# Kernel tuning notes

Hardware: AMD Instinct MI355X
Metric: run time of the kernel (lower is better)

The kernel has to match this reference:

```python
import jax, jax.numpy as jnp
import numpy as np

# --- static config (matches init_kwargs) ---
C = 384        # channels
H = 8          # num_heads
HD = C // H    # head_dim = 48
K = 1024       # patch_size (window)
BASE = 100.0   # rope_freq
MAX_POS = 4096
GRID_SIZE = 0.02
LN_EPS = 1e-5


def _interleave8(x, y, z):
    """Morton-interleave the low 8 bits of x,y,z -> 24-bit code (int32)."""
    key = jnp.zeros_like(x)
    for i in range(8):
        m = 1 << i
        key = key | ((x & m) << (2 * i + 2)) | ((y & m) << (2 * i + 1)) | ((z & m) << (2 * i))
    return key


def _serialize_points(xyz):
    """xyz: (B,3,N) -> (order (B,N) int32, grid (B,N,3) int32). Z-order sort."""
    pts = jnp.transpose(xyz, (0, 2, 1))                       # (B,N,3)
    grid = ((pts - pts.min(axis=1, keepdims=True)) / GRID_SIZE).astype(jnp.int32)
    grid = jnp.clip(grid, 0, 65535)
    gx, gy, gz = grid[..., 0], grid[..., 1], grid[..., 2]
    lo = _interleave8(gx & 255, gy & 255, gz & 255)           # low 24 bits of Morton code
    hi = _interleave8((gx >> 8) & 255, (gy >> 8) & 255, (gz >> 8) & 255)  # high word
    # 48-bit Morton order == lexsort with hi as primary key, lo secondary
    order = jax.vmap(lambda l, h: jnp.lexsort((l, h)))(lo, hi)
    return order.astype(jnp.int32), grid


def _rope_tables(d):
    inv_freq = 1.0 / (BASE ** (jnp.arange(0, d, 2, dtype=jnp.float32) / d))
    t = jnp.arange(MAX_POS, dtype=jnp.float32)
    freqs = t[:, None] * inv_freq[None, :]                    # (MAX_POS, d/2)
    freqs = jnp.concatenate([freqs, freqs], axis=-1)          # (MAX_POS, d)
    return jnp.cos(freqs), jnp.sin(freqs)


def _rotate_half(x):
    h = x.shape[-1] // 2
    return jnp.concatenate([-x[..., h:], x[..., :h]], axis=-1)


def _point_rope(tok, pos):
    """tok: (B,H,N,D) with D%3==0; pos: (B,N,3) int grid coords."""
    D = tok.shape[-1]
    d = D // 3
    pos = jnp.clip(pos, 0, MAX_POS - 1)
    cos, sin = _rope_tables(d)
    outs = []
    for axis, ch in enumerate(jnp.split(tok, 3, axis=-1)):
        p = pos[:, :, axis]                                   # (B,N)
        c = cos[p][:, None]                                   # (B,1,N,d)
        s = sin[p][:, None]
        outs.append(ch * c + _rotate_half(ch) * s)
    return jnp.concatenate(outs, axis=-1)


def _layernorm(x, g, b):
    mu = x.mean(axis=-1, keepdims=True)
    var = ((x - mu) ** 2).mean(axis=-1, keepdims=True)
    return (x - mu) * jax.lax.rsqrt(var + LN_EPS) * g + b


def _forward(x, xyz, ln1_g, ln1_b, qkv_w, qkv_b, proj_w, proj_b,
             ln2_g, ln2_b, ffn_w1, ffn_b1, ffn_w2, ffn_b2):
    B, C_, N = x.shape
    order, grid = _serialize_points(xyz)
    x_sorted = jnp.take_along_axis(x, order[:, None, :], axis=2)          # (B,C,N)
    grid_sorted = jnp.take_along_axis(grid, order[:, :, None], axis=1)    # (B,N,3)
    x_t = jnp.transpose(x_sorted, (0, 2, 1))                              # (B,N,C)
    shortcut = x_t
    xn = _layernorm(x_t, ln1_g, ln1_b)
    pad = (K - N % K) % K
    if pad > 0:
        xn = jnp.pad(xn, ((0, 0), (0, pad), (0, 0)))
        grid_sorted = jnp.pad(grid_sorted, ((0, 0), (0, pad), (0, 0)))
    Np = xn.shape[1]
    nw = Np // K
    qkv = (xn @ qkv_w + qkv_b).reshape(B, Np, 3, H, HD)
    q = jnp.transpose(qkv[:, :, 0], (0, 2, 1, 3))                         # (B,H,Np,HD)
    k = jnp.transpose(qkv[:, :, 1], (0, 2, 1, 3))
    v = jnp.transpose(qkv[:, :, 2], (0, 2, 1, 3))
    q = _point_rope(q, grid_sorted)
    k = _point_rope(k, grid_sorted)
    qw = q.reshape(B, H, nw, K, HD)
    kw = k.reshape(B, H, nw, K, HD)
    vw = v.reshape(B, H, nw, K, HD)
    scale = 1.0 / np.sqrt(HD).astype(np.float32)
    scores = jnp.einsum('bhwqd,bhwkd->bhwqk', qw, kw) * scale             # (B,H,nw,K,K)
    attn = jax.nn.softmax(scores, axis=-1)
    out = jnp.einsum('bhwqk,bhwkd->bhwqd', attn, vw)                      # (B,H,nw,K,HD)
    out = jnp.transpose(out, (0, 2, 3, 1, 4)).reshape(B, Np, C)
    out = out[:, :N]
    out = out @ proj_w + proj_b
    x_t = shortcut + out
    x_t = x_t + (jax.nn.gelu(_layernorm(x_t, ln2_g, ln2_b) @ ffn_w1 + ffn_b1,
                             approximate=False) @ ffn_w2 + ffn_b2)
    x_out = jnp.transpose(x_t, (0, 2, 1))                                 # (B,C,N)
    inv_order = jnp.argsort(order, axis=1)
    x_out = jnp.take_along_axis(x_out, inv_order[:, None, :], axis=2)
    return x_out


def setup_inputs() -> dict:
    key = jax.random.key(0)
    ks = jax.random.split(key, 12)
    B, N = 1, 16384
    s = 0.02
    return {
        'x': jax.random.normal(ks[0], (B, C, N), dtype=jnp.float32),
        'xyz': jax.random.uniform(ks[1], (B, 3, N), dtype=jnp.float32),
        'ln1_g': jnp.ones((C,), jnp.float32),
        'ln1_b': jnp.zeros((C,), jnp.float32),
        'qkv_w': jax.random.normal(ks[2], (C, 3 * C), jnp.float32) * s,
        'qkv_b': jnp.zeros((3 * C,), jnp.float32),
        'proj_w': jax.random.normal(ks[3], (C, C), jnp.float32) * s,
        'proj_b': jnp.zeros((C,), jnp.float32),
        'ln2_g': jnp.ones((C,), jnp.float32),
        'ln2_b': jnp.zeros((C,), jnp.float32),
        'ffn_w1': jax.random.normal(ks[4], (C, 4 * C), jnp.float32) * s,
        'ffn_b1': jnp.zeros((4 * C,), jnp.float32),
        'ffn_w2': jax.random.normal(ks[5], (4 * C, C), jnp.float32) * s,
        'ffn_b2': jnp.zeros((C,), jnp.float32),
    }


def reference(x, xyz, ln1_g, ln1_b, qkv_w, qkv_b, proj_w, proj_b,
              ln2_g, ln2_b, ffn_w1, ffn_b1, ffn_w2, ffn_b2):
    return _forward(x, xyz, ln1_g, ln1_b, qkv_w, qkv_b, proj_w, proj_b,
                    ln2_g, ln2_b, ffn_w1, ffn_b1, ffn_w2, ffn_b2)
```

## Files before the change

### kernel.cpp

```cpp
#include <hip/hip_runtime.h>
#include <hip/hip_bf16.h>

typedef unsigned short u16;
typedef unsigned int u32;
typedef unsigned long long u64;
typedef __attribute__((ext_vector_type(8))) short s16x8;
typedef __attribute__((ext_vector_type(4))) short s16x4;
typedef __attribute__((ext_vector_type(8))) unsigned short u16x8;
typedef __attribute__((ext_vector_type(4))) unsigned short u16x4;
typedef __attribute__((ext_vector_type(4))) float fx4;
typedef __attribute__((ext_vector_type(4))) unsigned int ux4;
typedef __attribute__((ext_vector_type(2))) unsigned int ux2;

__device__ __forceinline__ float bf2f(u16 u){ u32 x=((u32)u)<<16; return __builtin_bit_cast(float,x); }
__device__ __forceinline__ u16 f2bf(float f){ u32 x=__builtin_bit_cast(u32,f); return (u16)((x + 0x7FFFu + ((x>>16)&1u))>>16); }
__device__ __forceinline__ u32 cvtpk(float lo, float hi){
  u32 r; asm("v_cvt_pk_bf16_f32 %0, %1, %2" : "=v"(r) : "v"(lo), "v"(hi)); return r;
}

__device__ __forceinline__ s16x8 ld_bf8(const u16* p){
  s16x4 lo = *(const s16x4*)p;
  s16x4 hi = *(const s16x4*)(p+4);
  s16x8 r;
  r[0]=lo[0]; r[1]=lo[1]; r[2]=lo[2]; r[3]=lo[3];
  r[4]=hi[0]; r[5]=hi[1]; r[6]=hi[2]; r[7]=hi[3];
  return r;
}

__device__ __forceinline__ void gload16(const void* g, void* l){
  __builtin_amdgcn_global_load_lds((__attribute__((address_space(1))) void*)g,
                                   (__attribute__((address_space(3))) void*)l, 16, 0, 0);
}

__device__ __forceinline__ u64 spread3(u32 v){
  u64 x = v & 0xFFFFull;
  x = (x | (x<<32)) & 0x001f00000000ffffull;
  x = (x | (x<<16)) & 0x001f0000ff0000ffull;
  x = (x | (x<<8))  & 0x100f00f00f00f00full;
  x = (x | (x<<4))  & 0x10c30c30c30c30c3ull;
  x = (x | (x<<2))  & 0x1249249249249249ull;
  return x;
}

__global__ __launch_bounds__(256) void min3_kernel(const float* __restrict__ xyz, u32* __restrict__ mins, int N)
{
  int i = blockIdx.x*256 + threadIdx.x;
  float v0 = xyz[i], v1 = xyz[N+i], v2 = xyz[2*N+i];
  #pragma unroll
  for (int s=1;s<64;s<<=1){
    v0 = fminf(v0, __shfl_xor(v0,s));
    v1 = fminf(v1, __shfl_xor(v1,s));
    v2 = fminf(v2, __shfl_xor(v2,s));
  }
  if ((threadIdx.x & 63) == 0){
    atomicMin(mins+0, __builtin_bit_cast(u32, v0));
    atomicMin(mins+1, __builtin_bit_cast(u32, v1));
    atomicMin(mins+2, __builtin_bit_cast(u32, v2));
  }
}

__global__ __launch_bounds__(256) void keys_grid_kernel(const float* __restrict__ xyz, const u32* __restrict__ mins,
        u64* __restrict__ keys, int* __restrict__ gridO, int N)
{
  int i = blockIdx.x*256 + threadIdx.x;
  float mx0 = __builtin_bit_cast(float, mins[0]);
  float mx1 = __builtin_bit_cast(float, mins[1]);
  float mx2 = __builtin_bit_cast(float, mins[2]);
  int gx=(int)((xyz[i]-mx0)/0.02f);     gx = gx<0?0:(gx>65535?65535:gx);
  int gy=(int)((xyz[N+i]-mx1)/0.02f);   gy = gy<0?0:(gy>65535?65535:gy);
  int gz=(int)((xyz[2*N+i]-mx2)/0.02f); gz = gz<0?0:(gz>65535?65535:gz);
  gridO[i*3+0]=gx; gridO[i*3+1]=gy; gridO[i*3+2]=gz;
  u64 mort = (spread3((u32)gx)<<2)|(spread3((u32)gy)<<1)|spread3((u32)gz);
  keys[i] = (mort<<14) | (u64)i;
}

__global__ __launch_bounds__(1024) void bsort_kernel(u64* __restrict__ keys)
{
  __shared__ u64 sk[2048];
  int t = threadIdx.x;
  u64* base = keys + (size_t)blockIdx.x*2048;
  sk[t] = base[t]; sk[t+1024] = base[t+1024];
  for (int size=2; size<=2048; size<<=1){
    for (int stride=size>>1; stride>0; stride>>=1){
      __syncthreads();
      int i = 2*t - (t & (stride-1));
      int j = i + stride;
      u64 a = sk[i], b = sk[j];
      bool up = ((i & size) == 0);
      if ((a > b) == up){ sk[i]=b; sk[j]=a; }
    }
  }
  __syncthreads();
  base[t] = sk[t]; base[t+1024] = sk[t+1024];
}

template<bool FINAL>
__global__ __launch_bounds__(256) void merge_kernel(const u64* __restrict__ src, u64* __restrict__ dst,
        int* __restrict__ order, int L, int N)
{
  int gt = blockIdx.x*256 + threadIdx.x;
  int d0 = gt*8;
  if (d0 >= N) return;
  int pair = d0 / (2*L);
  int base = pair*2*L;
  int ld = d0 - base;
  const u64* A = src + base;
  const u64* B = A + L;
  int lo = ld > L ? ld - L : 0;
  int hi = ld < L ? ld : L;
  while (lo < hi){
    int mid = (lo+hi)>>1;
    if (A[mid] <= B[ld-1-mid]) lo = mid+1; else hi = mid;
  }
  int i = lo, j = ld - lo;
  u64* out = dst + base + ld;
  int* oout = order + base + ld;
  u64 a = (i < L) ? A[i] : ~0ull;
  u64 b = (j < L) ? B[j] : ~0ull;
  #pragma unroll
  for (int e=0;e<8;e++){
    u64 v;
    if (a <= b){ v = a; i++; a = (i<L)?A[i]:~0ull; }
    else       { v = b; j++; b = (j<L)?B[j]:~0ull; }
    out[e] = v;
    if (FINAL) oout[e] = (int)(v & 16383ull);
  }
}

__global__ __launch_bounds__(256) void wtrans4_kernel(const float* __restrict__ qkv_w, const float* __restrict__ proj_w,
    const float* __restrict__ w1, const float* __restrict__ w2,
    u16* __restrict__ qkv_wT, u16* __restrict__ proj_wT, u16* __restrict__ w1T, u16* __restrict__ w2T)
{
  __shared__ float tl[32][33];
  int bid = blockIdx.x;
  const float* W; u16* Wt; int K, Nc, lb;
  if (bid < 432)      { W=qkv_w;  Wt=qkv_wT;  K=384;  Nc=1152; lb=bid; }
  else if (bid < 576) { W=proj_w; Wt=proj_wT; K=384;  Nc=384;  lb=bid-432; }
  else if (bid < 1152){ W=w1;     Wt=w1T;     K=384;  Nc=1536; lb=bid-576; }
  else                { W=w2;     Wt=w2T;     K=1536; Nc=384;  lb=bid-1152; }
  int nb = Nc/32;
  int n0 = (lb % nb)*32;
  int k0 = (lb / nb)*32;
  int t=threadIdx.x; int r=t>>5, c=t&31;
  #pragma unroll
  for (int p=0;p<4;p++) tl[p*8+r][c] = W[(size_t)(k0+p*8+r)*Nc + n0+c];
  __syncthreads();
  #pragma unroll
  for (int p=0;p<4;p++) Wt[(size_t)(n0+p*8+r)*K + k0+c] = f2bf(tl[c][p*8+r]);
}

__global__ __launch_bounds__(256) void ln32_kernel(const float* __restrict__ x, const float* __restrict__ g,
     const float* __restrict__ b, u16* __restrict__ xn, int N)
{
  extern __shared__ char dsm[];
  float* tile = (float*)dsm;
  int n0 = blockIdx.x*32;
  int t = threadIdx.x;
  int tok32 = t&31, cg = t>>5;
  #pragma unroll 8
  for (int p=0;p<48;p++){
    int cc = p*8 + cg;
    tile[tok32*388 + cc] = x[(size_t)cc*N + n0 + tok32];
  }
  __syncthreads();
  int tok = t>>3, part = t&7;
  const float* row = tile + tok*388 + part*48;
  float s=0.f;
  #pragma unroll
  for (int j=0;j<48;j++) s += row[j];
  s += __shfl_xor(s,1); s += __shfl_xor(s,2); s += __shfl_xor(s,4);
  float mu = s*(1.0f/384.0f);
  float vr=0.f;
  #pragma unroll
  for (int j=0;j<48;j++){ float d=row[j]-mu; vr += d*d; }
  vr += __shfl_xor(vr,1); vr += __shfl_xor(vr,2); vr += __shfl_xor(vr,4);
  float rs = rsqrtf(vr*(1.0f/384.0f) + 1e-5f);
  u16* dst = xn + (size_t)(n0+tok)*384 + part*48;
  #pragma unroll
  for (int q=0;q<6;q++){
    float v[8];
    #pragma unroll
    for (int j=0;j<8;j++){
      int c = part*48 + q*8 + j;
      v[j] = (row[q*8+j]-mu)*rs*g[c] + b[c];
    }
    ux4 o;
    o[0]=cvtpk(v[0],v[1]); o[1]=cvtpk(v[2],v[3]); o[2]=cvtpk(v[4],v[5]); o[3]=cvtpk(v[6],v[7]);
    *(ux4*)(dst + q*8) = o;
  }
}

__device__ __forceinline__ float gelu_f(float v){
  return 0.5f*v*(1.0f + erff(v*0.7071067811865475f));
}

template<int EPI>
__global__ __launch_bounds__(256) void gemm128_kernel(const u16* __restrict__ A, const u16* __restrict__ Bt,
    const float* __restrict__ bias, u16* __restrict__ outB, float* __restrict__ outF,
    const float* __restrict__ res, int M, int Nout, int K)
{
  __shared__ u16 Al[128*64];
  __shared__ u16 Bl[128*64];
  int nmt = M>>7;
  int m0 = (blockIdx.x % nmt)<<7;
  int n0 = (blockIdx.x / nmt)<<7;
  int t = threadIdx.x, lane=t&63, wv=t>>6, wr=wv>>1, wc=wv&1;
  int fr = lane&15, fg = lane>>4;
  fx4 acc[4][4];
  #pragma unroll
  for (int i=0;i<4;i++)
  #pragma unroll
  for (int j=0;j<4;j++) acc[i][j]=(fx4){0.f,0.f,0.f,0.f};
  int srow = wv*32 + (lane>>3);
  int swz  = ((lane&7) ^ ((lane>>3)&7)) * 8;
  const u16* ApL = A  + (size_t)(m0+srow)*K + swz;
  const u16* BpL = Bt + (size_t)(n0+srow)*K + swz;
  u16* AlW = Al + wv*2048 + lane*8;
  u16* BlW = Bl + wv*2048 + lane*8;
  const u16* a_base = Al + (wr*64+fr)*64;
  const u16* b_base = Bl + (wc*64+fr)*64;
  int swr = fr & 7;
  for (int k0=0;k0<K;k0+=64){
    #pragma unroll
    for (int i=0;i<4;i++){
      gload16(ApL + k0 + (size_t)i*8*K, AlW + i*512);
      gload16(BpL + k0 + (size_t)i*8*K, BlW + i*512);
    }
    __syncthreads();
    #pragma unroll
    for (int ks=0;ks<2;ks++){
      int soff = (((ks*4+fg) ^ swr) << 3);
      s16x8 a[4], b[4];
      #pragma unroll
      for (int mi=0;mi<4;mi++) a[mi] = *(const s16x8*)(a_base + mi*1024 + soff);
      #pragma unroll
      for (int ni=0;ni<4;ni++) b[ni] = *(const s16x8*)(b_base + ni*1024 + soff);
      #pragma unroll
      for (int mi=0;mi<4;mi++)
      #pragma unroll
      for (int ni=0;ni<4;ni++)
        acc[mi][ni] = __builtin_amdgcn_mfma_f32_16x16x32_bf16(a[mi], b[ni], acc[mi][ni], 0,0,0);
    }
    __syncthreads();
  }
  if (EPI==0 || EPI==1){
    #pragma unroll
    for (int mi=0;mi<4;mi++)
    #pragma unroll
    for (int ni=0;ni<4;ni++){
      int c = n0 + wc*64 + ni*16 + fr;
      float bi = bias[c];
      int mb = m0 + wr*64 + mi*16 + fg*4;
      #pragma unroll
      for (int j=0;j<4;j++){
        float vv = acc[mi][ni][j] + bi;
        if (EPI==1) vv = gelu_f(vv);
        outB[(size_t)(mb+j)*Nout + c] = f2bf(vv);
      }
    }
  } else {
    #pragma unroll
    for (int mi=0;mi<4;mi++)
    #pragma unroll
    for (int ni=0;ni<4;ni++){
      int c = n0 + wc*64 + ni*16 + fr;
      float bi = bias[c];
      size_t idx = (size_t)c*M + m0 + wr*64 + mi*16 + fg*4;
      fx4 r4 = *(const fx4*)(res + idx);
      fx4 o;
      #pragma unroll
      for (int j=0;j<4;j++) o[j] = acc[mi][ni][j] + bi + r4[j];
      *(fx4*)(outF + idx) = o;
    }
  }
}

#define LOG2_100_O8 0.8304820237218405f

__global__ __launch_bounds__(256) void rope_kernel(const u16* __restrict__ qkv, const int* __restrict__ order,
    const int* __restrict__ gridO, u16* __restrict__ Qp, u16* __restrict__ Kp, u16* __restrict__ Vp, int N)
{
  __shared__ float csm[64][24][2];
  __shared__ int origs[64];
  int i0 = blockIdx.x<<6;
  int t = threadIdx.x;
  if (t<64) origs[t] = order[i0+t];
  __syncthreads();
  for (int idx=t; idx<64*24; idx+=256){
    int tok = idx/24, slot = idx - tok*24;
    int a = slot>>3, fi = slot&7;
    int pos = gridO[(size_t)origs[tok]*3 + a];
    pos = pos<0?0:(pos>4095?4095:pos);
    float invf = __builtin_amdgcn_exp2f(-(float)fi * LOG2_100_O8);
    float ang = (float)pos * invf;
    csm[tok][slot][0] = __cosf(ang);
    csm[tok][slot][1] = __sinf(ang);
  }
  __syncthreads();
  int tok = t&63;
  int i = i0 + tok;
  const u16* src = qkv + (size_t)origs[tok]*1152;
  for (int h=t>>6; h<8; h+=4){
    size_t dst = ((size_t)h*N + i)*48;
    #pragma unroll
    for (int a=0;a<3;a++){
      u16x8 qa = *(const u16x8*)(src + h*48 + a*16);
      u16x8 qb = *(const u16x8*)(src + h*48 + a*16 + 8);
      u16x8 ka = *(const u16x8*)(src + 384 + h*48 + a*16);
      u16x8 kb = *(const u16x8*)(src + 384 + h*48 + a*16 + 8);
      float oqa[8], oqb[8], oka[8], okb[8];
      #pragma unroll
      for (int j=0;j<8;j++){
        float c0 = csm[tok][a*8+j][0], s0 = csm[tok][a*8+j][1];
        float ql = bf2f(qa[j]), qh = bf2f(qb[j]);
        float kl = bf2f(ka[j]), kh = bf2f(kb[j]);
        oqa[j] = ql*c0 - qh*s0;
        oqb[j] = qh*c0 + ql*s0;
        oka[j] = kl*c0 - kh*s0;
        okb[j] = kh*c0 + kl*s0;
      }
      ux4 OQa, OQb, OKa, OKb;
      #pragma unroll
      for (int p=0;p<4;p++){
        OQa[p]=cvtpk(oqa[2*p],oqa[2*p+1]);
        OQb[p]=cvtpk(oqb[2*p],oqb[2*p+1]);
        OKa[p]=cvtpk(oka[2*p],oka[2*p+1]);
        OKb[p]=cvtpk(okb[2*p],okb[2*p+1]);
      }
      *(ux4*)(Qp + dst + a*16) = OQa;
      *(ux4*)(Qp + dst + a*16 + 8) = OQb;
      *(ux4*)(Kp + dst + a*16) = OKa;
      *(ux4*)(Kp + dst + a*16 + 8) = OKb;
      u16x8 va = *(const u16x8*)(src + 768 + h*48 + a*16);
      u16x8 vb = *(const u16x8*)(src + 768 + h*48 + a*16 + 8);
      *(u16x8*)(Vp + dst + a*16) = va;
      *(u16x8*)(Vp + dst + a*16 + 8) = vb;
    }
  }
}

#define ATTN_SCALE 0.14433756729740643f
#define E2SCALE 0.2082354550504211f
#define DEFER_RAW 55.0f
#define KSTRIDE 68

__global__ __launch_bounds__(512) void attn5_kernel(const u16* __restrict__ Qp, const u16* __restrict__ Kp,
    const u16* __restrict__ Vp, const int* __restrict__ order, u16* __restrict__ attn, int N, int nw)
{
  __shared__ u16 Kl[64*KSTRIDE];
  __shared__ u16 Vl[48*KSTRIDE];
  __shared__ u16 Pl[8][32*KSTRIDE];
  int b = blockIdx.x;
  int hw = b & 127;
  int qc = b >> 7;
  int w = hw % nw, h = hw / nw;
  int t = threadIdx.x, lane = t&63, wv = t>>6;
  int fr = lane & 15, fg = lane >> 4;
  size_t base = ((size_t)h*N + (size_t)w*1024);
  int q0 = qc*256 + wv*32;
  bool kact = t < 384;
  int krow = t/6, kc = t - krow*6;
  const u16* ksrc = Kp + (base + krow)*48 + kc*8;
  u16* kdst = Kl + krow*KSTRIDE + kc*8;
  int s2 = t - 128;
  bool vact = t >= 128;
  int vrow = s2/6, vc = s2 - vrow*6;
  const u16* vsrc = Vp + (base + vrow)*48 + vc*8;
  int vkey = vrow ^ (vc<<3);
  if (t < 256){ ux2 z = {0,0}; *(ux2*)&Kl[(t>>2)*KSTRIDE + 48 + (t&3)*4] = z; }
  s16x8 qf[2][2];
  s16x8 zf = {0,0,0,0,0,0,0,0};
  #pragma unroll
  for (int n=0;n<2;n++){
    const u16* qrow = Qp + (base + q0 + n*16 + fr)*48;
    qf[n][0] = ld_bf8(qrow + fg*8);
    qf[n][1] = (fg < 2) ? ld_bf8(qrow + 32 + fg*8) : zf;
  }

  float m0r = -3.4e38f, m1r = -3.4e38f;
  float ls0 = 0.f, ls1 = 0.f;
  fx4 o00=(fx4){0.f,0.f,0.f,0.f}, o01=o00, o02=o00, o10=o00, o11=o00, o12=o00;
  u16* pl = Pl[wv];
  ux4 kreg = {0,0,0,0}, vreg = {0,0,0,0};
  if (kact) kreg = *(const ux4*)ksrc;
  if (vact) vreg = *(const ux4*)vsrc;

  for (int c=0;c<16;c++){
    __syncthreads();
    if (kact){
      ux2 lo; lo[0]=kreg[0]; lo[1]=kreg[1];
      ux2 hi; hi[0]=kreg[2]; hi[1]=kreg[3];
      *(ux2*)kdst = lo; *(ux2*)(kdst+4) = hi;
    }
    if (vact){
      u16* vcp = Vl + vkey;
      vcp[(vc*8+0)*KSTRIDE] = (u16)vreg[0];
      vcp[(vc*8+1)*KSTRIDE] = (u16)(vreg[0]>>16);
      vcp[(vc*8+2)*KSTRIDE] = (u16)vreg[1];
      vcp[(vc*8+3)*KSTRIDE] = (u16)(vreg[1]>>16);
      vcp[(vc*8+4)*KSTRIDE] = (u16)vreg[2];
      vcp[(vc*8+5)*KSTRIDE] = (u16)(vreg[2]>>16);
      vcp[(vc*8+6)*KSTRIDE] = (u16)vreg[3];
      vcp[(vc*8+7)*KSTRIDE] = (u16)(vreg[3]>>16);
    }
    __syncthreads();
    if (c < 15){
      if (kact) kreg = *(const ux4*)(ksrc + (size_t)(c+1)*3072);
      if (vact) vreg = *(const ux4*)(vsrc + (size_t)(c+1)*3072);
    }
    fx4 s0[4], s1v[4];
    #pragma unroll
    for (int m=0;m<4;m++){
      s0[m]=(fx4){0.f,0.f,0.f,0.f}; s1v[m]=s0[m];
      #pragma unroll
      for (int s=0;s<2;s++){
        s16x8 af = ld_bf8(Kl + (m*16+fr)*KSTRIDE + s*32 + fg*8);
        s0[m]  = __builtin_amdgcn_mfma_f32_16x16x32_bf16(af, qf[0][s], s0[m],  0,0,0);
        s1v[m] = __builtin_amdgcn_mfma_f32_16x16x32_bf16(af, qf[1][s], s1v[m], 0,0,0);
      }
    }
    float pm0 = -3.4e38f, pm1 = -3.4e38f;
    #pragma unroll
    for (int m=0;m<4;m++)
    #pragma unroll
    for (int j=0;j<4;j++){ pm0 = fmaxf(pm0, s0[m][j]); pm1 = fmaxf(pm1, s1v[m][j]); }
    pm0 = fmaxf(pm0, __shfl_xor(pm0,16)); pm0 = fmaxf(pm0, __shfl_xor(pm0,32));
    pm1 = fmaxf(pm1, __shfl_xor(pm1,16)); pm1 = fmaxf(pm1, __shfl_xor(pm1,32));
    if (!__all((pm0 <= m0r + DEFER_RAW) & (pm1 <= m1r + DEFER_RAW))){
      float nm0 = fmaxf(m0r, pm0), nm1 = fmaxf(m1r, pm1);
      float f0 = __builtin_amdgcn_exp2f((m0r - nm0)*E2SCALE);
      float f1 = __builtin_amdgcn_exp2f((m1r - nm1)*E2SCALE);
      ls0 *= f0; ls1 *= f1;
      m0r = nm0; m1r = nm1;
      #pragma unroll
      for (int j=0;j<4;j++){
        float g0 = __shfl(f0, fg*4+j);
        float g1 = __shfl(f1, fg*4+j);
        o00[j]*=g0; o01[j]*=g0; o02[j]*=g0;
        o10[j]*=g1; o11[j]*=g1; o12[j]*=g1;
      }
    }
    #pragma unroll
    for (int m=0;m<4;m++){
      float e0[4], e1[4];
      #pragma unroll
      for (int j=0;j<4;j++){
        e0[j] = __builtin_amdgcn_exp2f((s0[m][j]-m0r)*E2SCALE);
        e1[j] = __builtin_amdgcn_exp2f((s1v[m][j]-m1r)*E2SCALE);
        ls0 += e0[j]; ls1 += e1[j];
      }
      ux2 P0, P1;
      P0[0]=cvtpk(e0[0],e0[1]); P0[1]=cvtpk(e0[2],e0[3]);
      P1[0]=cvtpk(e1[0],e1[1]); P1[1]=cvtpk(e1[2],e1[3]);
      *(ux2*)&pl[(fr)*KSTRIDE + m*16 + fg*4]      = P0;
      *(ux2*)&pl[(16+fr)*KSTRIDE + m*16 + fg*4]   = P1;
    }
    #pragma unroll
    for (int s=0;s<2;s++){
      s16x8 pa0 = ld_bf8(pl + fr*KSTRIDE + s*32 + fg*8);
      s16x8 pa1 = ld_bf8(pl + (16+fr)*KSTRIDE + s*32 + fg*8);
      int kb = s*32 + fg*8;
      s16x8 vb0 = ld_bf8(Vl + (fr)*KSTRIDE    + (kb ^ ((fr)&56)));
      s16x8 vb1 = ld_bf8(Vl + (16+fr)*KSTRIDE + (kb ^ ((16+fr)&56)));
      s16x8 vb2 = ld_bf8(Vl + (32+fr)*KSTRIDE + (kb ^ ((32+fr)&56)));
      o00 = __builtin_amdgcn_mfma_f32_16x16x32_bf16(pa0, vb0, o00, 0,0,0);
      o01 = __builtin_amdgcn_mfma_f32_16x16x32_bf16(pa0, vb1, o01, 0,0,0);
      o02 = __builtin_amdgcn_mfma_f32_16x16x32_bf16(pa0, vb2, o02, 0,0,0);
      o10 = __builtin_amdgcn_mfma_f32_16x16x32_bf16(pa1, vb0, o10, 0,0,0);
      o11 = __builtin_amdgcn_mfma_f32_16x16x32_bf16(pa1, vb1, o11, 0,0,0);
      o12 = __builtin_amdgcn_mfma_f32_16x16x32_bf16(pa1, vb2, o12, 0,0,0);
    }
  }
  ls0 += __shfl_xor(ls0,16); ls0 += __shfl_xor(ls0,32);
  ls1 += __shfl_xor(ls1,16); ls1 += __shfl_xor(ls1,32);
  float r0 = 1.0f/ls0, r1 = 1.0f/ls1;
  const int* ord = order + w*1024 + q0;
  #pragma unroll
  for (int j=0;j<4;j++){
    float inv0 = __shfl(r0, fg*4+j);
    float inv1 = __shfl(r1, fg*4+j);
    int orig0 = ord[fg*4+j];
    u16* dst0 = attn + (size_t)orig0*384 + h*48;
    dst0[fr]      = f2bf(o00[j]*inv0);
    dst0[16+fr]   = f2bf(o01[j]*inv0);
    dst0[32+fr]   = f2bf(o02[j]*inv0);
    int orig1 = ord[16 + fg*4+j];
    u16* dst1 = attn + (size_t)orig1*384 + h*48;
    dst1[fr]      = f2bf(o10[j]*inv1);
    dst1[16+fr]   = f2bf(o11[j]*inv1);
    dst1[32+fr]   = f2bf(o12[j]*inv1);
  }
}

extern "C" void kernel_launch(void* const* d_in, const int* in_sizes, int n_in,
                              void* d_out, int out_size, void* d_ws, size_t ws_size,
                              hipStream_t stream)
{
  (void)n_in; (void)out_size; (void)ws_size;
  const float* x     = (const float*)d_in[0];
  const float* xyz   = (const float*)d_in[1];
  const float* ln1_g = (const float*)d_in[2];
  const float* ln1_b = (const float*)d_in[3];
  const float* qkv_w = (const float*)d_in[4];
  const float* qkv_b = (const float*)d_in[5];
  const float* proj_w= (const float*)d_in[6];
  const float* proj_b= (const float*)d_in[7];
  const float* ln2_g = (const float*)d_in[8];
  const float* ln2_b = (const float*)d_in[9];
  const float* ffn_w1= (const float*)d_in[10];
  const float* ffn_b1= (const float*)d_in[11];
  const float* ffn_w2= (const float*)d_in[12];
  const float* ffn_b2= (const float*)d_in[13];
  int N = in_sizes[0]/384;
  int nw = N/1024;
  char* wsp = (char*)d_ws;
  size_t off = 0;
  auto alloc = [&](size_t bytes)->char*{ char* p = wsp + off; off = (off + bytes + 255) & ~(size_t)255; return p; };
  int*  order   = (int*)alloc((size_t)N*4);
  int*  gridO   = (int*)alloc((size_t)N*12);
  u32*  mins    = (u32*)alloc(256);
  u64*  keysA   = (u64*)alloc((size_t)N*8);
  u64*  keysB   = (u64*)alloc((size_t)N*8);
  u16*  qkv_wT  = (u16*)alloc((size_t)1152*384*2);
  u16*  proj_wT = (u16*)alloc((size_t)384*384*2);
  u16*  w1T     = (u16*)alloc((size_t)1536*384*2);
  u16*  w2T     = (u16*)alloc((size_t)384*1536*2);
  u16*  xn      = (u16*)alloc((size_t)N*384*2);
  u16*  Qp      = (u16*)alloc((size_t)N*48*8*2);
  u16*  Kp      = (u16*)alloc((size_t)N*48*8*2);
  u16*  Vp      = (u16*)alloc((size_t)N*48*8*2);
  u16*  qkvb    = (u16*)alloc((size_t)N*1152*2);
  float* y1     = (float*)alloc((size_t)N*384*4);
  u16*  attn    = xn;
  u16*  xn2     = qkvb;
  u16*  mid     = xn;
  float* outF = (float*)d_out;

  hipMemsetAsync(mins, 0xFF, 12, stream);
  min3_kernel<<<N/256, 256, 0, stream>>>(xyz, mins, N);
  keys_grid_kernel<<<N/256, 256, 0, stream>>>(xyz, mins, keysA, gridO, N);
  bsort_kernel<<<N/2048, 1024, 0, stream>>>(keysA);
  merge_kernel<false><<<N/2048, 256, 0, stream>>>(keysA, keysB, order, 2048, N);
  merge_kernel<false><<<N/2048, 256, 0, stream>>>(keysB, keysA, order, 4096, N);
  merge_kernel<true><<<N/2048, 256, 0, stream>>>(keysA, keysB, order, 8192, N);

  wtrans4_kernel<<<1728, 256, 0, stream>>>(qkv_w, proj_w, ffn_w1, ffn_w2, qkv_wT, proj_wT, w1T, w2T);
  ln32_kernel<<<N/32, 256, 32*388*4, stream>>>(x, ln1_g, ln1_b, xn, N);
  gemm128_kernel<0><<<(N/128)*(1152/128), 256, 0, stream>>>(xn, qkv_wT, qkv_b, qkvb, nullptr, nullptr, N, 1152, 384);
  rope_kernel<<<N/64, 256, 0, stream>>>(qkvb, order, gridO, Qp, Kp, Vp, N);
  attn5_kernel<<<8*nw*4, 512, 0, stream>>>(Qp, Kp, Vp, order, attn, N, nw);
  gemm128_kernel<2><<<(N/128)*(384/128), 256, 0, stream>>>(attn, proj_wT, proj_b, nullptr, y1, x, N, 384, 384);
  ln32_kernel<<<N/32, 256, 32*388*4, stream>>>(y1, ln2_g, ln2_b, xn2, N);
  gemm128_kernel<1><<<(N/128)*(1536/128), 256, 0, stream>>>(xn2, w1T, ffn_b1, mid, nullptr, nullptr, N, 1536, 384);
  gemm128_kernel<2><<<(N/128)*(384/128), 256, 0, stream>>>(mid, w2T, ffn_b2, nullptr, outF, y1, N, 384, 1536);
}
```

Baseline: 291.9 us.

## Fuse sort into cooperative kernel, pre-transpose V, store residual in bf16

Replaces the six sort-stage launches (memset, min, keys, bitonic, three merges) with one 8-block cooperative kernel that uses grid syncs. The rope kernel now writes V transposed per window, so attention loads V tiles with vector stores instead of scattered transposing LDS writes. The intermediate residual y1 is stored as bf16 rather than fp32, which halves its traffic but loses precision. s_setprio hints are added around the MFMA blocks. The merge stages now run on only 8 workgroups, which limits parallelism, and the strided transposed V writes in rope may be costly.

```diff
diff --git a/kernel.cpp b/kernel.cpp
--- a/kernel.cpp
+++ b/kernel.cpp
@@ -1,5 +1,8 @@
 #include <hip/hip_runtime.h>
 #include <hip/hip_bf16.h>
+#include <hip/hip_cooperative_groups.h>
+
+namespace cg = cooperative_groups;
 
 typedef unsigned short u16;
 typedef unsigned int u32;
@@ -42,65 +45,10 @@
   return x;
 }
 
-__global__ __launch_bounds__(256) void min3_kernel(const float* __restrict__ xyz, u32* __restrict__ mins, int N)
-{
-  int i = blockIdx.x*256 + threadIdx.x;
-  float v0 = xyz[i], v1 = xyz[N+i], v2 = xyz[2*N+i];
-  #pragma unroll
-  for (int s=1;s<64;s<<=1){
-    v0 = fminf(v0, __shfl_xor(v0,s));
-    v1 = fminf(v1, __shfl_xor(v1,s));
-    v2 = fminf(v2, __shfl_xor(v2,s));
-  }
-  if ((threadIdx.x & 63) == 0){
-    atomicMin(mins+0, __builtin_bit_cast(u32, v0));
-    atomicMin(mins+1, __builtin_bit_cast(u32, v1));
-    atomicMin(mins+2, __builtin_bit_cast(u32, v2));
-  }
-}
-
-__global__ __launch_bounds__(256) void keys_grid_kernel(const float* __restrict__ xyz, const u32* __restrict__ mins,
-        u64* __restrict__ keys, int* __restrict__ gridO, int N)
-{
-  int i = blockIdx.x*256 + threadIdx.x;
-  float mx0 = __builtin_bit_cast(float, mins[0]);
-  float mx1 = __builtin_bit_cast(float, mins[1]);
-  float mx2 = __builtin_bit_cast(float, mins[2]);
-  int gx=(int)((xyz[i]-mx0)/0.02f);     gx = gx<0?0:(gx>65535?65535:gx);
-  int gy=(int)((xyz[N+i]-mx1)/0.02f);   gy = gy<0?0:(gy>65535?65535:gy);
-  int gz=(int)((xyz[2*N+i]-mx2)/0.02f); gz = gz<0?0:(gz>65535?65535:gz);
-  gridO[i*3+0]=gx; gridO[i*3+1]=gy; gridO[i*3+2]=gz;
-  u64 mort = (spread3((u32)gx)<<2)|(spread3((u32)gy)<<1)|spread3((u32)gz);
-  keys[i] = (mort<<14) | (u64)i;
-}
-
-__global__ __launch_bounds__(1024) void bsort_kernel(u64* __restrict__ keys)
-{
-  __shared__ u64 sk[2048];
-  int t = threadIdx.x;
-  u64* base = keys + (size_t)blockIdx.x*2048;
-  sk[t] = base[t]; sk[t+1024] = base[t+1024];
-  for (int size=2; size<=2048; size<<=1){
-    for (int stride=size>>1; stride>0; stride>>=1){
-      __syncthreads();
-      int i = 2*t - (t & (stride-1));
-      int j = i + stride;
-      u64 a = sk[i], b = sk[j];
-      bool up = ((i & size) == 0);
-      if ((a > b) == up){ sk[i]=b; sk[j]=a; }
-    }
-  }
-  __syncthreads();
-  base[t] = sk[t]; base[t+1024] = sk[t+1024];
-}
-
-template<bool FINAL>
-__global__ __launch_bounds__(256) void merge_kernel(const u64* __restrict__ src, u64* __restrict__ dst,
-        int* __restrict__ order, int L, int N)
-{
-  int gt = blockIdx.x*256 + threadIdx.x;
-  int d0 = gt*8;
-  if (d0 >= N) return;
+__device__ __forceinline__ void merge2(const u64* __restrict__ src, u64* __restrict__ dst,
+        int* __restrict__ order, int L, int gt)
+{
+  int d0 = gt*2;
   int pair = d0 / (2*L);
   int base = pair*2*L;
   int ld = d0 - base;
@@ -113,18 +61,72 @@
     if (A[mid] <= B[ld-1-mid]) lo = mid+1; else hi = mid;
   }
   int i = lo, j = ld - lo;
-  u64* out = dst + base + ld;
-  int* oout = order + base + ld;
-  u64 a = (i < L) ? A[i] : ~0ull;
-  u64 b = (j < L) ? B[j] : ~0ull;
-  #pragma unroll
-  for (int e=0;e<8;e++){
+  #pragma unroll
+  for (int e=0;e<2;e++){
+    u64 a = (i < L) ? A[i] : ~0ull;
+    u64 b = (j < L) ? B[j] : ~0ull;
     u64 v;
-    if (a <= b){ v = a; i++; a = (i<L)?A[i]:~0ull; }
-    else       { v = b; j++; b = (j<L)?B[j]:~0ull; }
-    out[e] = v;
-    if (FINAL) oout[e] = (int)(v & 16383ull);
-  }
+    if (a <= b){ v = a; i++; } else { v = b; j++; }
+    dst[base+ld+e] = v;
+    if (order) order[base+ld+e] = (int)(v & 16383ull);
+  }
+}
+
+__global__ __launch_bounds__(1024) void sortc_kernel(const float* __restrict__ xyz,
+    float* __restrict__ minsW, u64* __restrict__ keysA, u64* __restrict__ keysB,
+    int* __restrict__ order, int* __restrict__ gridO, int N)
+{
+  cg::grid_group gg = cg::this_grid();
+  __shared__ u64 sk[2048];
+  __shared__ float red[3][16];
+  int t = threadIdx.x, bid = blockIdx.x;
+  int lane = t&63, wv = t>>6;
+  float m0=3.4e38f,m1=3.4e38f,m2=3.4e38f;
+  for (int i = bid*1024 + t; i < N; i += 8192){
+    m0=fminf(m0,xyz[i]); m1=fminf(m1,xyz[N+i]); m2=fminf(m2,xyz[2*N+i]);
+  }
+  #pragma unroll
+  for (int s=1;s<64;s<<=1){
+    m0=fminf(m0,__shfl_xor(m0,s));
+    m1=fminf(m1,__shfl_xor(m1,s));
+    m2=fminf(m2,__shfl_xor(m2,s));
+  }
+  if (lane==0){ red[0][wv]=m0; red[1][wv]=m1; red[2][wv]=m2; }
+  __syncthreads();
+  if (t<3){ float m=red[t][0]; for(int i=1;i<16;i++) m=fminf(m,red[t][i]); minsW[bid*3+t]=m; }
+  gg.sync();
+  float mn0=minsW[0], mn1=minsW[1], mn2=minsW[2];
+  for (int bb=1;bb<8;bb++){
+    mn0=fminf(mn0,minsW[bb*3+0]); mn1=fminf(mn1,minsW[bb*3+1]); mn2=fminf(mn2,minsW[bb*3+2]);
+  }
+  for (int i = bid*2048 + t; i < bid*2048 + 2048; i += 1024){
+    int gx=(int)((xyz[i]-mn0)/0.02f);     gx = gx<0?0:(gx>65535?65535:gx);
+    int gy=(int)((xyz[N+i]-mn1)/0.02f);   gy = gy<0?0:(gy>65535?65535:gy);
+    int gz=(int)((xyz[2*N+i]-mn2)/0.02f); gz = gz<0?0:(gz>65535?65535:gz);
+    gridO[i*3+0]=gx; gridO[i*3+1]=gy; gridO[i*3+2]=gz;
+    u64 mort = (spread3((u32)gx)<<2)|(spread3((u32)gy)<<1)|spread3((u32)gz);
+    sk[i - bid*2048] = (mort<<14) | (u64)i;
+  }
+  for (int size=2; size<=2048; size<<=1){
+    for (int stride=size>>1; stride>0; stride>>=1){
+      __syncthreads();
+      int i = 2*t - (t & (stride-1));
+      int j = i + stride;
+      u64 a = sk[i], b = sk[j];
+      bool up = ((i & size) == 0);
+      if ((a > b) == up){ sk[i]=b; sk[j]=a; }
+    }
+  }
+  __syncthreads();
+  keysA[bid*2048 + t] = sk[t];
+  keysA[bid*2048 + 1024 + t] = sk[t+1024];
+  gg.sync();
+  int gt = bid*1024 + t;
+  merge2(keysA, keysB, nullptr, 2048, gt);
+  gg.sync();
+  merge2(keysB, keysA, nullptr, 4096, gt);
+  gg.sync();
+  merge2(keysA, keysB, order, 8192, gt);
 }
 
 __global__ __launch_bounds__(256) void wtrans4_kernel(const float* __restrict__ qkv_w, const float* __restrict__ proj_w,
@@ -149,18 +151,22 @@
   for (int p=0;p<4;p++) Wt[(size_t)(n0+p*8+r)*K + k0+c] = f2bf(tl[c][p*8+r]);
 }
 
-__global__ __launch_bounds__(256) void ln32_kernel(const float* __restrict__ x, const float* __restrict__ g,
+template<bool BF16IN>
+__global__ __launch_bounds__(256) void ln32_kernel(const void* __restrict__ xin, const float* __restrict__ g,
      const float* __restrict__ b, u16* __restrict__ xn, int N)
 {
   extern __shared__ char dsm[];
   float* tile = (float*)dsm;
   int n0 = blockIdx.x*32;
   int t = threadIdx.x;
-  int tok32 = t&31, cg = t>>5;
+  int tok32 = t&31, cg2 = t>>5;
   #pragma unroll 8
   for (int p=0;p<48;p++){
-    int cc = p*8 + cg;
-    tile[tok32*388 + cc] = x[(size_t)cc*N + n0 + tok32];
+    int cc = p*8 + cg2;
+    float v;
+    if (BF16IN) v = bf2f(((const u16*)xin)[(size_t)cc*N + n0 + tok32]);
+    else        v = ((const float*)xin)[(size_t)cc*N + n0 + tok32];
+    tile[tok32*388 + cc] = v;
   }
   __syncthreads();
   int tok = t>>3, part = t&7;
@@ -197,7 +203,7 @@
 template<int EPI>
 __global__ __launch_bounds__(256) void gemm128_kernel(const u16* __restrict__ A, const u16* __restrict__ Bt,
     const float* __restrict__ bias, u16* __restrict__ outB, float* __restrict__ outF,
-    const float* __restrict__ res, int M, int Nout, int K)
+    const float* __restrict__ resF, const u16* __restrict__ resB, int M, int Nout, int K)
 {
   __shared__ u16 Al[128*64];
   __shared__ u16 Bl[128*64];
@@ -258,7 +264,7 @@
         outB[(size_t)(mb+j)*Nout + c] = f2bf(vv);
       }
     }
-  } else {
+  } else if (EPI==2){
     #pragma unroll
     for (int mi=0;mi<4;mi++)
     #pragma unroll
@@ -266,10 +272,26 @@
       int c = n0 + wc*64 + ni*16 + fr;
       float bi = bias[c];
       size_t idx = (size_t)c*M + m0 + wr*64 + mi*16 + fg*4;
-      fx4 r4 = *(const fx4*)(res + idx);
+      fx4 r4 = *(const fx4*)(resF + idx);
+      ux2 p;
+      p[0] = cvtpk(acc[mi][ni][0]+bi+r4[0], acc[mi][ni][1]+bi+r4[1]);
+      p[1] = cvtpk(acc[mi][ni][2]+bi+r4[2], acc[mi][ni][3]+bi+r4[3]);
+      *(ux2*)(outB + idx) = p;
+    }
+  } else {
+    #pragma unroll
+    for (int mi=0;mi<4;mi++)
+    #pragma unroll
+    for (int ni=0;ni<4;ni++){
+      int c = n0 + wc*64 + ni*16 + fr;
+      float bi = bias[c];
+      size_t idx = (size_t)c*M + m0 + wr*64 + mi*16 + fg*4;
+      ux2 rb = *(const ux2*)(resB + idx);
       fx4 o;
-      #pragma unroll
-      for (int j=0;j<4;j++) o[j] = acc[mi][ni][j] + bi + r4[j];
+      o[0] = acc[mi][ni][0] + bi + bf2f((u16)rb[0]);
+      o[1] = acc[mi][ni][1] + bi + bf2f((u16)(rb[0]>>16));
+      o[2] = acc[mi][ni][2] + bi + bf2f((u16)rb[1]);
+      o[3] = acc[mi][ni][3] + bi + bf2f((u16)(rb[1]>>16));
       *(fx4*)(outF + idx) = o;
     }
   }
@@ -278,11 +300,12 @@
 #define LOG2_100_O8 0.8304820237218405f
 
 __global__ __launch_bounds__(256) void rope_kernel(const u16* __restrict__ qkv, const int* __restrict__ order,
-    const int* __restrict__ gridO, u16* __restrict__ Qp, u16* __restrict__ Kp, u16* __restrict__ Vp, int N)
+    const int* __restrict__ gridO, u16* __restrict__ Qp, u16* __restrict__ Kp, u16* __restrict__ Vt, int N)
 {
   __shared__ float csm[64][24][2];
   __shared__ int origs[64];
   int i0 = blockIdx.x<<6;
+  int nw = N>>10;
   int t = threadIdx.x;
   if (t<64) origs[t] = order[i0+t];
   __syncthreads();
@@ -299,9 +322,12 @@
   __syncthreads();
   int tok = t&63;
   int i = i0 + tok;
+  int wdx = i >> 10;
+  int kw = i & 1023;
   const u16* src = qkv + (size_t)origs[tok]*1152;
   for (int h=t>>6; h<8; h+=4){
     size_t dst = ((size_t)h*N + i)*48;
+    u16* vt = Vt + (((size_t)h*nw + wdx)*48)*1024 + kw;
     #pragma unroll
     for (int a=0;a<3;a++){
       u16x8 qa = *(const u16x8*)(src + h*48 + a*16);
@@ -333,8 +359,11 @@
       *(ux4*)(Kp + dst + a*16 + 8) = OKb;
       u16x8 va = *(const u16x8*)(src + 768 + h*48 + a*16);
       u16x8 vb = *(const u16x8*)(src + 768 + h*48 + a*16 + 8);
-      *(u16x8*)(Vp + dst + a*16) = va;
-      *(u16x8*)(Vp + dst + a*16 + 8) = vb;
+      #pragma unroll
+      for (int j=0;j<8;j++){
+        vt[(size_t)(a*16+j)*1024]   = va[j];
+        vt[(size_t)(a*16+8+j)*1024] = vb[j];
+      }
     }
   }
 }
@@ -344,8 +373,8 @@
 #define DEFER_RAW 55.0f
 #define KSTRIDE 68
 
-__global__ __launch_bounds__(512) void attn5_kernel(const u16* __restrict__ Qp, const u16* __restrict__ Kp,
-    const u16* __restrict__ Vp, const int* __restrict__ order, u16* __restrict__ attn, int N, int nw)
+__global__ __launch_bounds__(512) void attn6_kernel(const u16* __restrict__ Qp, const u16* __restrict__ Kp,
+    const u16* __restrict__ Vt, const int* __restrict__ order, u16* __restrict__ attn, int N, int nw)
 {
   __shared__ u16 Kl[64*KSTRIDE];
   __shared__ u16 Vl[48*KSTRIDE];
@@ -357,6 +386,7 @@
   int t = threadIdx.x, lane = t&63, wv = t>>6;
   int fr = lane & 15, fg = lane >> 4;
   size_t base = ((size_t)h*N + (size_t)w*1024);
+  size_t vbase = ((size_t)h*nw + w)*48;
   int q0 = qc*256 + wv*32;
   bool kact = t < 384;
   int krow = t/6, kc = t - krow*6;
@@ -364,9 +394,9 @@
   u16* kdst = Kl + krow*KSTRIDE + kc*8;
   int s2 = t - 128;
   bool vact = t >= 128;
-  int vrow = s2/6, vc = s2 - vrow*6;
-  const u16* vsrc = Vp + (base + vrow)*48 + vc*8;
-  int vkey = vrow ^ (vc<<3);
+  int vrow = s2>>3, vcg = (s2&7)*8;
+  const u16* vsrc = Vt + (vbase + vrow)*1024 + vcg;
+  u16* vdst = Vl + vrow*KSTRIDE + vcg;
   if (t < 256){ ux2 z = {0,0}; *(ux2*)&Kl[(t>>2)*KSTRIDE + 48 + (t&3)*4] = z; }
   s16x8 qf[2][2];
   s16x8 zf = {0,0,0,0,0,0,0,0};
@@ -393,22 +423,17 @@
       *(ux2*)kdst = lo; *(ux2*)(kdst+4) = hi;
     }
     if (vact){
-      u16* vcp = Vl + vkey;
-      vcp[(vc*8+0)*KSTRIDE] = (u16)vreg[0];
-      vcp[(vc*8+1)*KSTRIDE] = (u16)(vreg[0]>>16);
-      vcp[(vc*8+2)*KSTRIDE] = (u16)vreg[1];
-      vcp[(vc*8+3)*KSTRIDE] = (u16)(vreg[1]>>16);
-      vcp[(vc*8+4)*KSTRIDE] = (u16)vreg[2];
-      vcp[(vc*8+5)*KSTRIDE] = (u16)(vreg[2]>>16);
-      vcp[(vc*8+6)*KSTRIDE] = (u16)vreg[3];
-      vcp[(vc*8+7)*KSTRIDE] = (u16)(vreg[3]>>16);
+      ux2 lo; lo[0]=vreg[0]; lo[1]=vreg[1];
+      ux2 hi; hi[0]=vreg[2]; hi[1]=vreg[3];
+      *(ux2*)vdst = lo; *(ux2*)(vdst+4) = hi;
     }
     __syncthreads();
     if (c < 15){
       if (kact) kreg = *(const ux4*)(ksrc + (size_t)(c+1)*3072);
-      if (vact) vreg = *(const ux4*)(vsrc + (size_t)(c+1)*3072);
+      if (vact) vreg = *(const ux4*)(vsrc + (size_t)(c+1)*64);
     }
     fx4 s0[4], s1v[4];
+    __builtin_amdgcn_s_setprio(1);
     #pragma unroll
     for (int m=0;m<4;m++){
       s0[m]=(fx4){0.f,0.f,0.f,0.f}; s1v[m]=s0[m];
@@ -419,11 +444,14 @@
         s1v[m] = __builtin_amdgcn_mfma_f32_16x16x32_bf16(af, qf[1][s], s1v[m], 0,0,0);
       }
     }
+    __builtin_amdgcn_s_setprio(0);
     float pm0 = -3.4e38f, pm1 = -3.4e38f;
     #pragma unroll
-    for (int m=0;m<4;m++)
-    #pragma unroll
-    for (int j=0;j<4;j++){ pm0 = fmaxf(pm0, s0[m][j]); pm1 = fmaxf(pm1, s1v[m][j]); }
+    for (int m=0;m<4;m++){
+      float a0 = fmaxf(fmaxf(s0[m][0],s0[m][1]), fmaxf(s0[m][2],s0[m][3]));
+      float a1 = fmaxf(fmaxf(s1v[m][0],s1v[m][1]), fmaxf(s1v[m][2],s1v[m][3]));
+      pm0 = fmaxf(pm0, a0); pm1 = fmaxf(pm1, a1);
+    }
     pm0 = fmaxf(pm0, __shfl_xor(pm0,16)); pm0 = fmaxf(pm0, __shfl_xor(pm0,32));
     pm1 = fmaxf(pm1, __shfl_xor(pm1,16)); pm1 = fmaxf(pm1, __shfl_xor(pm1,32));
     if (!__all((pm0 <= m0r + DEFER_RAW) & (pm1 <= m1r + DEFER_RAW))){
@@ -455,14 +483,15 @@
       *(ux2*)&pl[(fr)*KSTRIDE + m*16 + fg*4]      = P0;
       *(ux2*)&pl[(16+fr)*KSTRIDE + m*16 + fg*4]   = P1;
     }
+    __builtin_amdgcn_s_setprio(1);
     #pragma unroll
     for (int s=0;s<2;s++){
-      s16x8 pa0 = ld_bf8(pl + fr*KSTRIDE + s*32 + fg*8);
-      s16x8 pa1 = ld_bf8(pl + (16+fr)*KSTRIDE + s*32 + fg*8);
       int kb = s*32 + fg*8;
-      s16x8 vb0 = ld_bf8(Vl + (fr)*KSTRIDE    + (kb ^ ((fr)&56)));
-      s16x8 vb1 = ld_bf8(Vl + (16+fr)*KSTRIDE + (kb ^ ((16+fr)&56)));
-      s16x8 vb2 = ld_bf8(Vl + (32+fr)*KSTRIDE + (kb ^ ((32+fr)&56)));
+      s16x8 pa0 = ld_bf8(pl + fr*KSTRIDE + kb);
+      s16x8 pa1 = ld_bf8(pl + (16+fr)*KSTRIDE + kb);
+      s16x8 vb0 = ld_bf8(Vl + (fr)*KSTRIDE    + kb);
+      s16x8 vb1 = ld_bf8(Vl + (16+fr)*KSTRIDE + kb);
+      s16x8 vb2 = ld_bf8(Vl + (32+fr)*KSTRIDE + kb);
       o00 = __builtin_amdgcn_mfma_f32_16x16x32_bf16(pa0, vb0, o00, 0,0,0);
       o01 = __builtin_amdgcn_mfma_f32_16x16x32_bf16(pa0, vb1, o01, 0,0,0);
       o02 = __builtin_amdgcn_mfma_f32_16x16x32_bf16(pa0, vb2, o02, 0,0,0);
@@ -470,6 +499,7 @@
       o11 = __builtin_amdgcn_mfma_f32_16x16x32_bf16(pa1, vb1, o11, 0,0,0);
       o12 = __builtin_amdgcn_mfma_f32_16x16x32_bf16(pa1, vb2, o12, 0,0,0);
     }
+    __builtin_amdgcn_s_setprio(0);
   }
   ls0 += __shfl_xor(ls0,16); ls0 += __shfl_xor(ls0,32);
   ls1 += __shfl_xor(ls1,16); ls1 += __shfl_xor(ls1,32);
@@ -518,7 +548,7 @@
   auto alloc = [&](size_t bytes)->char*{ char* p = wsp + off; off = (off + bytes + 255) & ~(size_t)255; return p; };
   int*  order   = (int*)alloc((size_t)N*4);
   int*  gridO   = (int*)alloc((size_t)N*12);
-  u32*  mins    = (u32*)alloc(256);
+  float* minsW  = (float*)alloc(256);
   u64*  keysA   = (u64*)alloc((size_t)N*8);
   u64*  keysB   = (u64*)alloc((size_t)N*8);
   u16*  qkv_wT  = (u16*)alloc((size_t)1152*384*2);
@@ -528,29 +558,29 @@
   u16*  xn      = (u16*)alloc((size_t)N*384*2);
   u16*  Qp      = (u16*)alloc((size_t)N*48*8*2);
   u16*  Kp      = (u16*)alloc((size_t)N*48*8*2);
-  u16*  Vp      = (u16*)alloc((size_t)N*48*8*2);
+  u16*  Vt      = (u16*)alloc((size_t)N*48*8*2);
   u16*  qkvb    = (u16*)alloc((size_t)N*1152*2);
-  float* y1     = (float*)alloc((size_t)N*384*4);
+  u16*  y1b     = (u16*)alloc((size_t)N*384*2);
   u16*  attn    = xn;
   u16*  xn2     = qkvb;
   u16*  mid     = xn;
   float* outF = (float*)d_out;
 
-  hipMemsetAsync(mins, 0xFF, 12, stream);
-  min3_kernel<<<N/256, 256, 0, stream>>>(xyz, mins, N);
-  keys_grid_kernel<<<N/256, 256, 0, stream>>>(xyz, mins, keysA, gridO, N);
-  bsort_kernel<<<N/2048, 1024, 0, stream>>>(keysA);
-  merge_kernel<false><<<N/2048, 256, 0, stream>>>(keysA, keysB, order, 2048, N);
-  merge_kernel<false><<<N/2048, 256, 0, stream>>>(keysB, keysA, order, 4096, N);
-  merge_kernel<true><<<N/2048, 256, 0, stream>>>(keysA, keysB, order, 8192, N);
+  {
+    const float* xyzp = xyz;
+    int Nv = N;
+    void* sargs[] = { (void*)&xyzp, (void*)&minsW, (void*)&keysA, (void*)&keysB,
+                      (void*)&order, (void*)&gridO, (void*)&Nv };
+    hipLaunchCooperativeKernel((const void*)sortc_kernel, dim3(8), dim3(1024), sargs, 0, stream);
+  }
 
   wtrans4_kernel<<<1728, 256, 0, stream>>>(qkv_w, proj_w, ffn_w1, ffn_w2, qkv_wT, proj_wT, w1T, w2T);
-  ln32_kernel<<<N/32, 256, 32*388*4, stream>>>(x, ln1_g, ln1_b, xn, N);
-  gemm128_kernel<0><<<(N/128)*(1152/128), 256, 0, stream>>>(xn, qkv_wT, qkv_b, qkvb, nullptr, nullptr, N, 1152, 384);
-  rope_kernel<<<N/64, 256, 0, stream>>>(qkvb, order, gridO, Qp, Kp, Vp, N);
-  attn5_kernel<<<8*nw*4, 512, 0, stream>>>(Qp, Kp, Vp, order, attn, N, nw);
-  gemm128_kernel<2><<<(N/128)*(384/128), 256, 0, stream>>>(attn, proj_wT, proj_b, nullptr, y1, x, N, 384, 384);
-  ln32_kernel<<<N/32, 256, 32*388*4, stream>>>(y1, ln2_g, ln2_b, xn2, N);
-  gemm128_kernel<1><<<(N/128)*(1536/128), 256, 0, stream>>>(xn2, w1T, ffn_b1, mid, nullptr, nullptr, N, 1536, 384);
-  gemm128_kernel<2><<<(N/128)*(384/128), 256, 0, stream>>>(mid, w2T, ffn_b2, nullptr, outF, y1, N, 384, 1536);
-}
+  ln32_kernel<false><<<N/32, 256, 32*388*4, stream>>>(x, ln1_g, ln1_b, xn, N);
+  gemm128_kernel<0><<<(N/128)*(1152/128), 256, 0, stream>>>(xn, qkv_wT, qkv_b, qkvb, nullptr, nullptr, nullptr, N, 1152, 384);
+  rope_kernel<<<N/64, 256, 0, stream>>>(qkvb, order, gridO, Qp, Kp, Vt, N);
+  attn6_kernel<<<8*nw*4, 512, 0, stream>>>(Qp, Kp, Vt, order, attn, N, nw);
+  gemm128_kernel<2><<<(N/128)*(384/128), 256, 0, stream>>>(attn, proj_wT, proj_b, y1b, nullptr, x, nullptr, N, 384, 384);
+  ln32_kernel<true><<<N/32, 256, 32*388*4, stream>>>(y1b, ln2_g, ln2_b, xn2, N);
+  gemm128_kernel<1><<<(N/128)*(1536/128), 256, 0, stream>>>(xn2, w1T, ffn_b1, mid, nullptr, nullptr, nullptr, N, 1536, 384);
+  gemm128_kernel<3><<<(N/128)*(384/128), 256, 0, stream>>>(mid, w2T, ffn_b2, nullptr, outF, nullptr, y1b, N, 384, 1536);
+}
```

Result: slower. 303.2 us (median of 2 runs) (+3.9%).
